# Optimization experiments

Hardware: AMD Instinct MI355X
Metric: run time of the kernel (lower is better)

## Reference

```python
import jax, jax.numpy as jnp
import numpy as np

N = 50000
E = 400000
IN_FEATS = 512
HEADS = 8
OUT_FEATS = 64
NEG_SLOPE = 0.2


def setup_inputs() -> dict:
    key = jax.random.key(0)
    ks = jax.random.split(key, 12)
    HF = HEADS * OUT_FEATS
    s = 1.0 / np.sqrt(IN_FEATS)
    inp = {
        "feat": jax.random.normal(ks[0], (N, IN_FEATS), dtype=jnp.float32),
        "src": jax.random.randint(ks[1], (E,), 0, N, dtype=jnp.int32),
        "dst": jax.random.randint(ks[2], (E,), 0, N, dtype=jnp.int32),
        "W_src": jax.random.normal(ks[3], (IN_FEATS, HF), dtype=jnp.float32) * s,
        "b_src": jax.random.normal(ks[4], (HF,), dtype=jnp.float32) * 0.01,
        "W_dst": jax.random.normal(ks[5], (IN_FEATS, HF), dtype=jnp.float32) * s,
        "b_dst": jax.random.normal(ks[6], (HF,), dtype=jnp.float32) * 0.01,
        "W_val": jax.random.normal(ks[7], (IN_FEATS, HF), dtype=jnp.float32) * s,
        "b_val": jax.random.normal(ks[8], (HF,), dtype=jnp.float32) * 0.01,
        "attn_l": jax.random.normal(ks[9], (HEADS, OUT_FEATS), dtype=jnp.float32) * 0.1,
        "attn_r": jax.random.normal(ks[10], (HEADS, OUT_FEATS), dtype=jnp.float32) * 0.1,
    }
    return inp


def reference(feat, src, dst, W_src, b_src, W_dst, b_dst, W_val, b_val, attn_l, attn_r):
    # node projections: [N, H, F]
    feat_src = (feat @ W_src + b_src).reshape(N, HEADS, OUT_FEATS)
    feat_dst = (feat @ W_dst + b_dst).reshape(N, HEADS, OUT_FEATS)
    feat_v = (feat @ W_val + b_val).reshape(N, HEADS, OUT_FEATS)

    # per-node attention logits: [N, H]
    el = jnp.einsum("nhf,hf->nh", feat_src, attn_l)
    er = jnp.einsum("nhf,hf->nh", feat_dst, attn_r)

    # per-edge logits with leaky relu: [E, H]
    e = el[src] + er[dst]
    e = jnp.where(e >= 0, e, NEG_SLOPE * e)

    # edge softmax segmented by destination node
    e_max = jax.ops.segment_max(e, dst, num_segments=N)  # [N, H]
    e_max = jnp.where(jnp.isfinite(e_max), e_max, 0.0)
    exp_e = jnp.exp(e - e_max[dst])  # [E, H]
    denom = jax.ops.segment_sum(exp_e, dst, num_segments=N)  # [N, H]
    a = exp_e / jnp.maximum(denom[dst], 1e-16)  # [E, H]

    # weighted gather-scatter aggregation: [N, H, F]
    msg = feat_v[src] * a[:, :, None]
    rst = jax.ops.segment_sum(msg, dst, num_segments=N)
    return rst.reshape(N, HEADS * OUT_FEATS)
```

## Files before the change

kernel.cpp:

```cpp
#include <hip/hip_runtime.h>
#include <math.h>

constexpr int N_NODES = 50000;
constexpr int N_PAD   = 50048;
constexpr int N_EDGES = 400000;
constexpr int IN_F = 512;
constexpr int HEADS = 8;
constexpr int OUT_F = 64;
constexpr int HF = 512;
constexpr float NEG = 0.2f;

typedef __bf16 bf16x8 __attribute__((ext_vector_type(8)));
typedef float  f32x4  __attribute__((ext_vector_type(4)));

__device__ __forceinline__ unsigned short f2bf(float f) {
    unsigned u = __float_as_uint(f);
    u += 0x7fffu + ((u >> 16) & 1u);
    return (unsigned short)(u >> 16);
}
__device__ __forceinline__ unsigned packbf2(float lo, float hi) {
    return (unsigned)f2bf(lo) | ((unsigned)f2bf(hi) << 16);
}

constexpr int K14_HIST0 = 289;
constexpr int K14_BLOCKS = K14_HIST0 + (N_EDGES + 255) / 256;

__global__ __launch_bounds__(256) void k14_misc(
        const float* __restrict__ W_val, unsigned short* __restrict__ Wt,
        const float* __restrict__ W_src, const float* __restrict__ b_src,
        const float* __restrict__ W_dst, const float* __restrict__ b_dst,
        const float* __restrict__ attn_l, const float* __restrict__ attn_r,
        float* __restrict__ w_l, float* __restrict__ w_r,
        float* __restrict__ c_l, float* __restrict__ c_r,
        const int* __restrict__ dst, int* __restrict__ deg) {
    __shared__ float tile[32][33];
    int b = blockIdx.x, t = threadIdx.x;
    if (b < 256) {
        int bi = b >> 4, bj = b & 15;
        for (int i = t; i < 1024; i += 256) {
            int r = i >> 5, c = i & 31;
            tile[r][c] = W_val[(size_t)(bi * 32 + r) * HF + bj * 32 + c];
        }
        __syncthreads();
        for (int i = t; i < 1024; i += 256) {
            int r = i >> 5, c = i & 31;
            Wt[(size_t)(bj * 32 + r) * IN_F + bi * 32 + c] = f2bf(tile[c][r]);
        }
    } else if (b < K14_HIST0) {
        int gid = (b - 256) * 256 + t;
        if (gid < 4096) {
            int k = gid >> 3, h = gid & 7;
            float s = 0.f;
            #pragma unroll 8
            for (int f = 0; f < OUT_F; ++f) s += W_src[k * HF + h * OUT_F + f] * attn_l[h * OUT_F + f];
            w_l[k * 8 + h] = s;
        } else if (gid < 8192) {
            int g = gid - 4096;
            int k = g >> 3, h = g & 7;
            float s = 0.f;
            #pragma unroll 8
            for (int f = 0; f < OUT_F; ++f) s += W_dst[k * HF + h * OUT_F + f] * attn_r[h * OUT_F + f];
            w_r[k * 8 + h] = s;
        } else if (gid < 8192 + 16) {
            int g = gid - 8192;
            int h = g & 7;
            float s = 0.f;
            if (g < 8) {
                for (int f = 0; f < OUT_F; ++f) s += b_src[h * OUT_F + f] * attn_l[h * OUT_F + f];
                c_l[h] = s;
            } else {
                for (int f = 0; f < OUT_F; ++f) s += b_dst[h * OUT_F + f] * attn_r[h * OUT_F + f];
                c_r[h] = s;
            }
        }
    } else {
        int e = (b - K14_HIST0) * 256 + t;
        if (e < N_EDGES) atomicAdd(&deg[dst[e]], 1);
    }
}

constexpr int K0F_GRID = 1024;

__global__ __launch_bounds__(256, 2) void k0_fused(
        const float* __restrict__ feat,
        const float* __restrict__ w_l, const float* __restrict__ w_r,
        const float* __restrict__ c_l, const float* __restrict__ c_r,
        unsigned short* __restrict__ feat_bf,
        float* __restrict__ el, float* __restrict__ er) {
    __shared__ float4 lw[2048];
    int t = threadIdx.x;
    int lane = t & 63, wv = t >> 6;

    const float4* gl = (const float4*)w_l;
    const float4* gr = (const float4*)w_r;
    #pragma unroll
    for (int p = 0; p < 8; ++p) {
        int i = t + 256 * p;
        int sw = i ^ ((i >> 4) & 7);
        lw[sw] = (i < 1024) ? gl[i] : gr[i - 1024];
    }
    __syncthreads();

    float4 wl0[8], wl1[8], wr0[8], wr1[8];
    #pragma unroll
    for (int j = 0; j < 8; ++j) {
        int i0 = 16 * lane + 2 * j;
        wl0[j] = lw[i0 ^ ((i0 >> 4) & 7)];
        int i1 = i0 + 1;
        wl1[j] = lw[i1 ^ ((i1 >> 4) & 7)];
        int i2 = 1024 + i0;
        wr0[j] = lw[i2 ^ ((i2 >> 4) & 7)];
        int i3 = i2 + 1;
        wr1[j] = lw[i3 ^ ((i3 >> 4) & 7)];
    }

    int idx = ((lane & 1) << 3) | ((lane & 2) << 1) | ((lane & 4) >> 1) | ((lane & 8) >> 3);
    int oh = idx & 7, oside = idx >> 3;
    float cadd = 0.f;
    if (lane < 16) cadd = oside ? c_r[oh] : c_l[oh];

    const int NQ = N_NODES / 4;
    int q = blockIdx.x;
    if (q >= NQ) return;

    float4 f0, f1;
    {
        const float* fr = feat + (size_t)(q * 4 + wv) * IN_F + lane * 8;
        f0 = *(const float4*)fr;
        f1 = *(const float4*)(fr + 4);
    }

    while (true) {
        int qn = q + K0F_GRID;
        float4 n0, n1;
        if (qn < NQ) {
            const float* fr = feat + (size_t)(qn * 4 + wv) * IN_F + lane * 8;
            n0 = *(const float4*)fr;
            n1 = *(const float4*)(fr + 4);
        }

        int row = q * 4 + wv;
        uint4 vv;
        vv.x = packbf2(f0.x, f0.y); vv.y = packbf2(f0.z, f0.w);
        vv.z = packbf2(f1.x, f1.y); vv.w = packbf2(f1.z, f1.w);
        *(uint4*)(feat_bf + (size_t)row * IN_F + lane * 8) = vv;

        float v[16];
        #pragma unroll
        for (int c = 0; c < 16; ++c) v[c] = 0.f;
        float ff[8] = {f0.x, f0.y, f0.z, f0.w, f1.x, f1.y, f1.z, f1.w};
        #pragma unroll
        for (int j = 0; j < 8; ++j) {
            float f = ff[j];
            v[0]  = fmaf(f, wl0[j].x, v[0]);
            v[1]  = fmaf(f, wl0[j].y, v[1]);
            v[2]  = fmaf(f, wl0[j].z, v[2]);
            v[3]  = fmaf(f, wl0[j].w, v[3]);
            v[4]  = fmaf(f, wl1[j].x, v[4]);
            v[5]  = fmaf(f, wl1[j].y, v[5]);
            v[6]  = fmaf(f, wl1[j].z, v[6]);
            v[7]  = fmaf(f, wl1[j].w, v[7]);
            v[8]  = fmaf(f, wr0[j].x, v[8]);
            v[9]  = fmaf(f, wr0[j].y, v[9]);
            v[10] = fmaf(f, wr0[j].z, v[10]);
            v[11] = fmaf(f, wr0[j].w, v[11]);
            v[12] = fmaf(f, wr1[j].x, v[12]);
            v[13] = fmaf(f, wr1[j].y, v[13]);
            v[14] = fmaf(f, wr1[j].z, v[14]);
            v[15] = fmaf(f, wr1[j].w, v[15]);
        }

        #pragma unroll
        for (int j = 0; j < 8; ++j) {
            float a = v[j], b = v[j + 8];
            float send = (lane & 1) ? a : b;
            float recv = __shfl_xor(send, 1, 64);
            v[j] = ((lane & 1) ? b : a) + recv;
        }
        #pragma unroll
        for (int j = 0; j < 4; ++j) {
            float a = v[j], b = v[j + 4];
            float send = (lane & 2) ? a : b;
            float recv = __shfl_xor(send, 2, 64);
            v[j] = ((lane & 2) ? b : a) + recv;
        }
        #pragma unroll
        for (int j = 0; j < 2; ++j) {
            float a = v[j], b = v[j + 2];
            float send = (lane & 4) ? a : b;
            float recv = __shfl_xor(send, 4, 64);
            v[j] = ((lane & 4) ? b : a) + recv;
        }
        {
            float a = v[0], b = v[1];
            float send = (lane & 8) ? a : b;
            float recv = __shfl_xor(send, 8, 64);
            v[0] = ((lane & 8) ? b : a) + recv;
        }
        float tot = v[0];
        tot += __shfl_xor(tot, 16, 64);
        tot += __shfl_xor(tot, 32, 64);

        if (lane < 16) {
            float o = tot + cadd;
            if (oside) er[(size_t)row * 8 + oh] = o;
            else       el[(size_t)row * 8 + oh] = o;
        }

        if (qn >= NQ) break;
        q = qn; f0 = n0; f1 = n1;
    }
}

__global__ __launch_bounds__(1024) void kS_scan(const int* __restrict__ deg,
                                                int* __restrict__ offs,
                                                int* __restrict__ cursor) {
    __shared__ int wsum[16];
    __shared__ int base_s;
    int b = blockIdx.x, t = threadIdx.x;
    int lane = t & 63, wid = t >> 6;

    int pre = 0;
    for (int i = t; i < b * 1024; i += 1024) pre += deg[i];
    #pragma unroll
    for (int off = 32; off; off >>= 1) pre += __shfl_down(pre, (unsigned)off, 64);
    if (lane == 0) wsum[wid] = pre;
    __syncthreads();
    if (t == 0) {
        int s = 0;
        for (int i = 0; i < 16; ++i) s += wsum[i];
        base_s = s;
    }
    __syncthreads();
    int base = base_s;
    __syncthreads();

    int i = b * 1024 + t;
    int v = (i < N_NODES) ? deg[i] : 0;
    int x = v;
    #pragma unroll
    for (int off = 1; off < 64; off <<= 1) {
        int y = __shfl_up(x, (unsigned)off, 64);
        if (lane >= off) x += y;
    }
    if (lane == 63) wsum[wid] = x;
    __syncthreads();
    if (wid == 0) {
        int s = (lane < 16) ? wsum[lane] : 0;
        #pragma unroll
        for (int off = 1; off < 16; off <<= 1) {
            int y = __shfl_up(s, (unsigned)off, 64);
            if (lane >= off) s += y;
        }
        if (lane < 16) wsum[lane] = s;
    }
    __syncthreads();
    int woff = wid ? wsum[wid - 1] : 0;
    if (i < N_NODES) {
        int excl = base + woff + x - v;
        offs[i] = excl;
        cursor[i] = excl;
    }
}

__global__ __launch_bounds__(256) void k3_mfma(
        const unsigned short* __restrict__ Abf,
        const unsigned short* __restrict__ Bbf,
        const float* __restrict__ bias,
        unsigned short* __restrict__ C) {
    __shared__ unsigned short As[128 * 64];
    __shared__ unsigned short Bs[128 * 64];
    int tid = threadIdx.x;
    int w = tid >> 6, lane = tid & 63;
    int bm = blockIdx.x >> 2, bn = blockIdx.x & 3;
    int rowBase = bm * 128, colBase = bn * 128;
    int wm = w >> 1, wn = w & 1;
    int c15 = lane & 15, q = lane >> 4;

    f32x4 acc[4][4] = {};

    for (int k0 = 0; k0 < IN_F; k0 += 64) {
        #pragma unroll
        for (int rnd = 0; rnd < 4; ++rnd) {
            int e = w * 256 + rnd * 64 + lane;
            int r = e >> 3, p = e & 7;
            int lc = p ^ (r & 7);
            const unsigned short* gA = Abf + (size_t)(rowBase + r) * IN_F + k0 + lc * 8;
            unsigned short* lA = &As[(w * 256 + rnd * 64) * 8];
            __builtin_amdgcn_global_load_lds(
                (const __attribute__((address_space(1))) unsigned int*)gA,
                (__attribute__((address_space(3))) unsigned int*)lA, 16, 0, 0);
            const unsigned short* gB = Bbf + (size_t)(colBase + r) * IN_F + k0 + lc * 8;
            unsigned short* lB = &Bs[(w * 256 + rnd * 64) * 8];
            __builtin_amdgcn_global_load_lds(
                (const __attribute__((address_space(1))) unsigned int*)gB,
                (__attribute__((address_space(3))) unsigned int*)lB, 16, 0, 0);
        }
        __syncthreads();

        #pragma unroll
        for (int ks = 0; ks < 2; ++ks) {
            bf16x8 a[4], b[4];
            #pragma unroll
            for (int mi = 0; mi < 4; ++mi) {
                int row = wm * 64 + mi * 16 + c15;
                int pc = (ks * 4 + q) ^ (row & 7);
                a[mi] = *(const bf16x8*)&As[row * 64 + pc * 8];
            }
            #pragma unroll
            for (int nj = 0; nj < 4; ++nj) {
                int row = wn * 64 + nj * 16 + c15;
                int pc = (ks * 4 + q) ^ (row & 7);
                b[nj] = *(const bf16x8*)&Bs[row * 64 + pc * 8];
            }
            #pragma unroll
            for (int mi = 0; mi < 4; ++mi)
                #pragma unroll
                for (int nj = 0; nj < 4; ++nj)
                    acc[mi][nj] = __builtin_amdgcn_mfma_f32_16x16x32_bf16(
                        a[mi], b[nj], acc[mi][nj], 0, 0, 0);
        }
        __syncthreads();
    }

    #pragma unroll
    for (int nj = 0; nj < 4; ++nj) {
        int col = colBase + wn * 64 + nj * 16 + c15;
        float bv = bias[col];
        #pragma unroll
        for (int mi = 0; mi < 4; ++mi) {
            int row0 = rowBase + wm * 64 + mi * 16 + q * 4;
            #pragma unroll
            for (int rg = 0; rg < 4; ++rg) {
                C[(size_t)(row0 + rg) * HF + col] = f2bf(acc[mi][nj][rg] + bv);
            }
        }
    }
}

__global__ __launch_bounds__(256) void k6_scatter(
        const int* __restrict__ src, const int* __restrict__ dst,
        int* __restrict__ cursor, int* __restrict__ srcs) {
    int e = blockIdx.x * 256 + threadIdx.x;
    if (e < N_EDGES) {
        int pos = atomicAdd(&cursor[dst[e]], 1);
        srcs[pos] = src[e];
    }
}

__device__ __forceinline__ void accum8(float* acc, uint4 v, float w) {
    unsigned u;
    u = v.x;
    acc[0] = fmaf(w, __uint_as_float(u << 16), acc[0]);
    acc[1] = fmaf(w, __uint_as_float(u & 0xffff0000u), acc[1]);
    u = v.y;
    acc[2] = fmaf(w, __uint_as_float(u << 16), acc[2]);
    acc[3] = fmaf(w, __uint_as_float(u & 0xffff0000u), acc[3]);
    u = v.z;
    acc[4] = fmaf(w, __uint_as_float(u << 16), acc[4]);
    acc[5] = fmaf(w, __uint_as_float(u & 0xffff0000u), acc[5]);
    u = v.w;
    acc[6] = fmaf(w, __uint_as_float(u << 16), acc[6]);
    acc[7] = fmaf(w, __uint_as_float(u & 0xffff0000u), acc[7]);
}

__global__ __launch_bounds__(256) void k8_agg(
        const int* __restrict__ srcs, const int* __restrict__ offs,
        const int* __restrict__ deg,
        const float* __restrict__ el, const float* __restrict__ er,
        const uint4* __restrict__ feat_v,
        float* __restrict__ out) {
    int lane = threadIdx.x & 63;
    int n = blockIdx.x * 4 + (threadIdx.x >> 6);
    int start = offs[n], cnt = deg[n];
    int h = lane >> 3;
    float erh = er[(size_t)n * 8 + h];
    float acc[8] = {};
    float dsum = 0.f;

    for (int base = 0; base < cnt; base += 64) {
        int m = cnt - base; if (m > 64) m = 64;
        int s_all = (lane < m) ? srcs[start + base + lane] : 0;
        int i = 0;
        for (; i + 8 <= m; i += 8) {
            int s[8]; uint4 v[8]; float e[8];
            #pragma unroll
            for (int j = 0; j < 8; ++j) s[j] = __shfl(s_all, i + j, 64);
            #pragma unroll
            for (int j = 0; j < 8; ++j) v[j] = feat_v[(size_t)s[j] * 64 + lane];
            #pragma unroll
            for (int j = 0; j < 8; ++j) e[j] = el[(size_t)s[j] * 8 + h];
            #pragma unroll
            for (int j = 0; j < 8; ++j) {
                float x = e[j] + erh;
                x = (x >= 0.f) ? x : NEG * x;
                float w = __expf(x);
                dsum += w;
                accum8(acc, v[j], w);
            }
        }
        for (; i < m; ++i) {
            int s0 = __shfl(s_all, i, 64);
            uint4 v0 = feat_v[(size_t)s0 * 64 + lane];
            float x = el[(size_t)s0 * 8 + h] + erh;
            x = (x >= 0.f) ? x : NEG * x;
            float w = __expf(x);
            dsum += w;
            accum8(acc, v0, w);
        }
    }

    float dn = 1.f / fmaxf(dsum, 1e-16f);
    float* op = out + (size_t)n * HF + lane * 8;
    *(float4*)op       = make_float4(acc[0] * dn, acc[1] * dn, acc[2] * dn, acc[3] * dn);
    *(float4*)(op + 4) = make_float4(acc[4] * dn, acc[5] * dn, acc[6] * dn, acc[7] * dn);
}

extern "C" void kernel_launch(void* const* d_in, const int* in_sizes, int n_in,
                              void* d_out, int out_size, void* d_ws, size_t ws_size,
                              hipStream_t stream) {
    const float* feat   = (const float*)d_in[0];
    const int*   src    = (const int*)d_in[1];
    const int*   dst    = (const int*)d_in[2];
    const float* W_src  = (const float*)d_in[3];
    const float* b_src  = (const float*)d_in[4];
    const float* W_dst  = (const float*)d_in[5];
    const float* b_dst  = (const float*)d_in[6];
    const float* W_val  = (const float*)d_in[7];
    const float* b_val  = (const float*)d_in[8];
    const float* attn_l = (const float*)d_in[9];
    const float* attn_r = (const float*)d_in[10];
    float* out = (float*)d_out;

    char* ws = (char*)d_ws;
    size_t off = 0;
    auto alloc = [&](size_t bytes) -> void* {
        void* p = ws + off;
        off += (bytes + 255) & ~(size_t)255;
        return p;
    };

    unsigned short* feat_bf = (unsigned short*)alloc((size_t)N_PAD * IN_F * 2);
    unsigned short* Wt      = (unsigned short*)alloc((size_t)IN_F * HF * 2);
    unsigned short* feat_v  = (unsigned short*)alloc((size_t)N_PAD * HF * 2);
    float* w_l    = (float*)alloc(4096 * 4);
    float* w_r    = (float*)alloc(4096 * 4);
    float* c_l    = (float*)alloc(8 * 4);
    float* c_r    = (float*)alloc(8 * 4);
    float* el     = (float*)alloc((size_t)N_NODES * 8 * 4);
    float* er     = (float*)alloc((size_t)N_NODES * 8 * 4);
    int*   deg    = (int*)alloc((size_t)N_NODES * 4);
    int*   offs   = (int*)alloc((size_t)N_NODES * 4);
    int*   cursor = (int*)alloc((size_t)N_NODES * 4);
    int*   srcs   = (int*)alloc((size_t)N_EDGES * 4);
    (void)ws_size; (void)in_sizes; (void)n_in; (void)out_size;

    hipMemsetAsync(deg, 0, (size_t)N_NODES * 4, stream);
    k14_misc<<<K14_BLOCKS, 256, 0, stream>>>(W_val, Wt, W_src, b_src, W_dst, b_dst,
                                             attn_l, attn_r, w_l, w_r, c_l, c_r, dst, deg);
    k0_fused<<<K0F_GRID, 256, 0, stream>>>(feat, w_l, w_r, c_l, c_r, feat_bf, el, er);
    kS_scan<<<(N_NODES + 1023) / 1024, 1024, 0, stream>>>(deg, offs, cursor);
    k3_mfma<<<(N_PAD / 128) * 4, 256, 0, stream>>>(feat_bf, Wt, b_val, feat_v);
    k6_scatter<<<(N_EDGES + 255) / 256, 256, 0, stream>>>(src, dst, cursor, srcs);
    k8_agg<<<N_NODES / 4, 256, 0, stream>>>(srcs, offs, deg, el, er,
                                            (const uint4*)feat_v, out);
}
```

Before: 377.5 us.

## Split aggregation by head with persistent blocks and per-lane edge weights

The aggregation kernel now assigns each block one attention head and loops persistently over node chunks. Each lane computes the exp weight for one edge and the weights are broadcast by shuffle, so the kernel no longer evaluates exp redundantly per 8-lane group. The denominator is reduced across the wave. Each lane now gathers one 2-byte bf16 value instead of a 16-byte vector, giving narrower, less coalesced gathers and re-reading the src indices and degrees once per head, in exchange for more parallelism and less ALU work per edge.

```diff
diff --git a/kernel.cpp b/kernel.cpp
--- a/kernel.cpp
+++ b/kernel.cpp
@@ -348,72 +348,62 @@
     }
 }
 
-__device__ __forceinline__ void accum8(float* acc, uint4 v, float w) {
-    unsigned u;
-    u = v.x;
-    acc[0] = fmaf(w, __uint_as_float(u << 16), acc[0]);
-    acc[1] = fmaf(w, __uint_as_float(u & 0xffff0000u), acc[1]);
-    u = v.y;
-    acc[2] = fmaf(w, __uint_as_float(u << 16), acc[2]);
-    acc[3] = fmaf(w, __uint_as_float(u & 0xffff0000u), acc[3]);
-    u = v.z;
-    acc[4] = fmaf(w, __uint_as_float(u << 16), acc[4]);
-    acc[5] = fmaf(w, __uint_as_float(u & 0xffff0000u), acc[5]);
-    u = v.w;
-    acc[6] = fmaf(w, __uint_as_float(u << 16), acc[6]);
-    acc[7] = fmaf(w, __uint_as_float(u & 0xffff0000u), acc[7]);
-}
-
-__global__ __launch_bounds__(256) void k8_agg(
+constexpr int K8_BLOCKS = 2048;
+constexpr int K8_CHUNK_STRIDE = K8_BLOCKS / 8;
+
+__global__ __launch_bounds__(256, 8) void k8_agg(
         const int* __restrict__ srcs, const int* __restrict__ offs,
         const int* __restrict__ deg,
         const float* __restrict__ el, const float* __restrict__ er,
-        const uint4* __restrict__ feat_v,
+        const unsigned short* __restrict__ feat_v,
         float* __restrict__ out) {
     int lane = threadIdx.x & 63;
-    int n = blockIdx.x * 4 + (threadIdx.x >> 6);
-    int start = offs[n], cnt = deg[n];
-    int h = lane >> 3;
-    float erh = er[(size_t)n * 8 + h];
-    float acc[8] = {};
-    float dsum = 0.f;
-
-    for (int base = 0; base < cnt; base += 64) {
-        int m = cnt - base; if (m > 64) m = 64;
-        int s_all = (lane < m) ? srcs[start + base + lane] : 0;
-        int i = 0;
-        for (; i + 8 <= m; i += 8) {
-            int s[8]; uint4 v[8]; float e[8];
-            #pragma unroll
-            for (int j = 0; j < 8; ++j) s[j] = __shfl(s_all, i + j, 64);
-            #pragma unroll
-            for (int j = 0; j < 8; ++j) v[j] = feat_v[(size_t)s[j] * 64 + lane];
-            #pragma unroll
-            for (int j = 0; j < 8; ++j) e[j] = el[(size_t)s[j] * 8 + h];
-            #pragma unroll
-            for (int j = 0; j < 8; ++j) {
-                float x = e[j] + erh;
-                x = (x >= 0.f) ? x : NEG * x;
-                float w = __expf(x);
-                dsum += w;
-                accum8(acc, v[j], w);
-            }
-        }
-        for (; i < m; ++i) {
-            int s0 = __shfl(s_all, i, 64);
-            uint4 v0 = feat_v[(size_t)s0 * 64 + lane];
-            float x = el[(size_t)s0 * 8 + h] + erh;
+    int wv = threadIdx.x >> 6;
+    int head = blockIdx.x & 7;
+    const unsigned short* fvh = feat_v + head * OUT_F;
+
+    for (int chunk = (blockIdx.x >> 3); chunk < N_NODES / 4; chunk += K8_CHUNK_STRIDE) {
+        int n = chunk * 4 + wv;
+        int start = offs[n], cnt = deg[n];
+        float erh = er[(size_t)n * 8 + head];
+        float acc = 0.f;
+        float dsum = 0.f;
+
+        for (int base = 0; base < cnt; base += 64) {
+            int m = cnt - base; if (m > 64) m = 64;
+            int s_all = (lane < m) ? srcs[start + base + lane] : 0;
+            float x = el[(size_t)s_all * 8 + head] + erh;
             x = (x >= 0.f) ? x : NEG * x;
-            float w = __expf(x);
-            dsum += w;
-            accum8(acc, v0, w);
-        }
-    }
-
-    float dn = 1.f / fmaxf(dsum, 1e-16f);
-    float* op = out + (size_t)n * HF + lane * 8;
-    *(float4*)op       = make_float4(acc[0] * dn, acc[1] * dn, acc[2] * dn, acc[3] * dn);
-    *(float4*)(op + 4) = make_float4(acc[4] * dn, acc[5] * dn, acc[6] * dn, acc[7] * dn);
+            float w_ln = __expf(x);
+            if (lane < m) dsum += w_ln;
+
+            int i = 0;
+            for (; i + 8 <= m; i += 8) {
+                int s[8]; unsigned short v[8]; float wj[8];
+                #pragma unroll
+                for (int j = 0; j < 8; ++j) s[j] = __shfl(s_all, i + j, 64);
+                #pragma unroll
+                for (int j = 0; j < 8; ++j) v[j] = fvh[(size_t)s[j] * HF + lane];
+                #pragma unroll
+                for (int j = 0; j < 8; ++j) wj[j] = __shfl(w_ln, i + j, 64);
+                #pragma unroll
+                for (int j = 0; j < 8; ++j)
+                    acc = fmaf(wj[j], __uint_as_float(((unsigned)v[j]) << 16), acc);
+            }
+            for (; i < m; ++i) {
+                int s0 = __shfl(s_all, i, 64);
+                unsigned short v0 = fvh[(size_t)s0 * HF + lane];
+                float w0 = __shfl(w_ln, i, 64);
+                acc = fmaf(w0, __uint_as_float(((unsigned)v0) << 16), acc);
+            }
+        }
+
+        #pragma unroll
+        for (int off = 1; off < 64; off <<= 1) dsum += __shfl_xor(dsum, off, 64);
+
+        float dn = 1.f / fmaxf(dsum, 1e-16f);
+        out[(size_t)n * HF + head * OUT_F + lane] = acc * dn;
+    }
 }
 
 extern "C" void kernel_launch(void* const* d_in, const int* in_sizes, int n_in,
@@ -462,6 +452,5 @@
     kS_scan<<<(N_NODES + 1023) / 1024, 1024, 0, stream>>>(deg, offs, cursor);
     k3_mfma<<<(N_PAD / 128) * 4, 256, 0, stream>>>(feat_bf, Wt, b_val, feat_v);
     k6_scatter<<<(N_EDGES + 255) / 256, 256, 0, stream>>>(src, dst, cursor, srcs);
-    k8_agg<<<N_NODES / 4, 256, 0, stream>>>(srcs, offs, deg, el, er,
-                                            (const uint4*)feat_v, out);
-}
+    k8_agg<<<K8_BLOCKS, 256, 0, stream>>>(srcs, offs, deg, el, er, feat_v, out);
+}
```

New measurement: 468.1 us. 24.0% more time.
